# Performance work log

Hardware: AMD Instinct MI355X
Metric: run time of the kernel (lower is better)

The kernel has to match this reference:

```python
import jax, jax.numpy as jnp
import numpy as np

N, E, F_IN, H, C = 10000, 320000, 256, 256, 40


def setup_inputs() -> dict:
    key = jax.random.key(0)
    ks = jax.random.split(key, 12)
    inp = {
        "x": jax.random.normal(ks[0], (N, F_IN), dtype=jnp.float32),
        "edge_index": jax.random.randint(ks[1], (2, E), 0, N, dtype=jnp.int64),
    }
    dims = [(F_IN, H), (H, H), (H, H), (H, H), (H, C)]
    for i, (din, dout) in enumerate(dims, start=1):
        scale = 1.0 / np.sqrt(din)
        inp[f"W{i}"] = jax.random.normal(ks[1 + i], (din, dout), dtype=jnp.float32) * scale
        inp[f"b{i}"] = jnp.zeros((dout,), dtype=jnp.float32)
    return inp


def _gcn_norm(edge_index, num_nodes, dtype):
    # GCNConv: add self-loops, symmetric normalization D^-1/2 (A+I) D^-1/2
    loops = jnp.arange(num_nodes, dtype=edge_index.dtype)
    src = jnp.concatenate([edge_index[0], loops])
    dst = jnp.concatenate([edge_index[1], loops])
    deg = jax.ops.segment_sum(jnp.ones_like(dst, dtype=dtype), dst, num_segments=num_nodes)
    dinv = jnp.where(deg > 0, deg ** -0.5, 0.0).astype(dtype)
    norm = dinv[src] * dinv[dst]  # [E+N]
    return src, dst, norm


def _conv(h, src, dst, norm, W, b, num_nodes):
    # linear transform then gather-scale-scatter aggregation
    h = h @ W                           # [N, dout]
    msg = h[src] * norm[:, None]        # [E+N, dout]
    return jax.ops.segment_sum(msg, dst, num_segments=num_nodes) + b


def reference(x, edge_index, W1, b1, W2, b2, W3, b3, W4, b4, W5, b5):
    num_nodes = x.shape[0]
    src, dst, norm = _gcn_norm(edge_index, num_nodes, x.dtype)
    h = jax.nn.relu(_conv(x, src, dst, norm, W1, b1, num_nodes))
    h = jax.nn.relu(_conv(h, src, dst, norm, W2, b2, num_nodes))
    h = jax.nn.relu(_conv(h, src, dst, norm, W3, b3, num_nodes))
    h = jax.nn.relu(_conv(h, src, dst, norm, W4, b4, num_nodes))
    logits = _conv(h, src, dst, norm, W5, b5, num_nodes)
    return jax.nn.log_softmax(logits, axis=1), logits
```

## Files before the change

kernel.cpp:

```cpp
#include <hip/hip_runtime.h>
#include <hip/hip_bf16.h>

#define N_NODES 10000
#define N_EDGES 320000
#define HDIM    256
#define NCLS    40
#define WTOT    273448

typedef __attribute__((ext_vector_type(8))) short short8;
typedef __attribute__((ext_vector_type(4))) float floatx4;
typedef unsigned long long ull;
typedef unsigned short ushort;

__device__ __forceinline__ float bf2f(ushort u) {
    union { unsigned int i; float f; } v; v.i = ((unsigned int)u) << 16; return v.f;
}
__device__ __forceinline__ ushort f2bf(float f) {
    __hip_bfloat16 h = __float2bfloat16(f);
    return *reinterpret_cast<ushort*>(&h);
}

__device__ __forceinline__ void detect_flags(const void* x, const void* ei,
                                             int* sflags) {
    const int tid = threadIdx.x;
    if (tid < 64) {
        const ushort* u = (const ushort*)x;
        int e = (u[2 * tid] >> 7) & 0xFF;
        ull badmask = __ballot(e < 100 || e > 140);
        const int* ii = (const int*)ei;
        ull oddnz = __ballot(ii[2 * tid + 1] != 0);
        if (tid == 0) {
            sflags[0] = (__popcll(badmask) >= 8) ? 1 : 0;
            sflags[1] = (oddnz == 0) ? 1 : 0;
        }
    }
    __syncthreads();
}


struct PrepArgs {
    const void* x;
    const void* ei;
    const void* wsrc[10];
    ushort* wdst[10];
    int woffs[11];
    ushort* xb;
    int* src32;
    int* dst32;
    int* cnt;
    ushort* tbuf;
    ushort* hbuf;
    int* flags;
};

#define PREP_XB 2500
#define PREP_WB 1069
#define PREP_EB 1250
#define PREP_TOTAL (PREP_XB + PREP_WB + PREP_EB + 1)

__global__ __launch_bounds__(256)
void prep_kernel(PrepArgs a) {
    __shared__ int sflags[2];
    detect_flags(a.x, a.ei, sflags);
    const int f32 = sflags[0];
    const int b = blockIdx.x;

    if (b < PREP_XB) {
        int i4 = b * 256 + threadIdx.x;
        if (f32) {
            float4 v = ((const float4*)a.x)[i4];
            ull p = (ull)f2bf(v.x) | ((ull)f2bf(v.y) << 16) |
                    ((ull)f2bf(v.z) << 32) | ((ull)f2bf(v.w) << 48);
            ((ull*)a.xb)[i4] = p;
        } else {
            ((ull*)a.xb)[i4] = ((const ull*)a.x)[i4];
        }
    } else if (b < PREP_XB + PREP_WB) {
        int i = (b - PREP_XB) * 256 + threadIdx.x;
        if (i < WTOT) {
            int t = 0;
#pragma unroll
            for (int k = 1; k < 10; ++k) t += (i >= a.woffs[k]);
            int local = i - a.woffs[t];
            ushort v;
            if (f32) v = f2bf(((const float*)a.wsrc[t])[local]);
            else     v = ((const ushort*)a.wsrc[t])[local];
            a.wdst[t][local] = v;
        }
    } else if (b < PREP_XB + PREP_WB + PREP_EB) {
        int e = (b - PREP_XB - PREP_WB) * 256 + threadIdx.x;
        const int* ii = (const int*)a.ei;
        int s, d;
        if (sflags[1]) { s = ii[2 * e]; d = ii[2 * (N_EDGES + e)]; }
        else           { s = ii[e];     d = ii[N_EDGES + e]; }
        s = ((unsigned)s < N_NODES) ? s : 0;
        d = ((unsigned)d < N_NODES) ? d : 0;
        a.src32[e] = s;
        a.dst32[e] = d;
        atomicAdd(&a.cnt[d], 1);
    } else {
        int t = threadIdx.x;
        if (t < 64)       ((ull*)(a.tbuf + (size_t)N_NODES * 256))[t] = 0;
        else if (t < 128) ((ull*)(a.hbuf + (size_t)N_NODES * 256))[t - 64] = 0;
        if (t == 0) { a.flags[0] = sflags[0]; a.flags[1] = sflags[1]; }
    }
}


__global__ __launch_bounds__(1024)
void scan_dinv_kernel(const int* __restrict__ cnt, int* __restrict__ offs,
                      int* __restrict__ woff, float* __restrict__ dinv) {
    __shared__ int part[1024];
    const int t = threadIdx.x;
    const int CH = (N_NODES + 1023) / 1024;
    const int base = t * CH;
    int s = 0;
    for (int j = 0; j < CH; ++j) {
        int i = base + j;
        if (i < N_NODES) s += cnt[i];
    }
    part[t] = s;
    __syncthreads();
    for (int off = 1; off < 1024; off <<= 1) {
        int v = 0;
        if (t >= off) v = part[t - off];
        __syncthreads();
        part[t] += v;
        __syncthreads();
    }
    int run = (t == 0) ? 0 : part[t - 1];
    for (int j = 0; j < CH; ++j) {
        int i = base + j;
        if (i < N_NODES) {
            int c = cnt[i];
            offs[i] = run;
            woff[i] = run;
            dinv[i] = rsqrtf((float)c + 1.0f);
            run += c;
        }
    }
}


#define FILL_BLKS 1250
#define GEMM1_YT  78
#define FG_TOTAL  (FILL_BLKS + 8 * GEMM1_YT)

__global__ __launch_bounds__(256)
void fillgemm_kernel(const int* __restrict__ src, const int* __restrict__ dst,
                     int* __restrict__ woff, int* __restrict__ csr,
                     const ushort* __restrict__ A, const ushort* __restrict__ W,
                     const float* __restrict__ dinv, ushort* __restrict__ T) {
    const int b = blockIdx.x;
    if (b < FILL_BLKS) {
        int e = b * 256 + threadIdx.x;
        int d = dst[e];
        int p = atomicAdd(&woff[d], 1);
        csr[p] = src[e];
        return;
    }
    const int g = b - FILL_BLKS;
    const int lane = threadIdx.x & 63;
    const int wave = threadIdx.x >> 6;
    const int m = lane & 15;
    const int quad = lane >> 4;
    const int c0 = (g & 7) * 32;
    const int by = g >> 3;

    short8 bfrag[2][8];
#pragma unroll
    for (int t = 0; t < 2; ++t)
#pragma unroll
        for (int s = 0; s < 8; ++s)
#pragma unroll
            for (int j = 0; j < 8; ++j)
                bfrag[t][s][j] = (short)W[(size_t)(s * 32 + quad * 8 + j) * 256 + c0 + t * 16 + m];

    const int step = GEMM1_YT * 4;
    for (int rt = by * 4 + wave; rt < N_NODES / 16; rt += step) {
        const int r0 = rt * 16;
        floatx4 acc0 = {0.f, 0.f, 0.f, 0.f};
        floatx4 acc1 = {0.f, 0.f, 0.f, 0.f};
        const ushort* arow = A + (size_t)(r0 + m) * 256 + quad * 8;
#pragma unroll
        for (int s = 0; s < 8; ++s) {
            short8 af = *(const short8*)(arow + s * 32);
            acc0 = __builtin_amdgcn_mfma_f32_16x16x32_bf16(af, bfrag[0][s], acc0, 0, 0, 0);
            acc1 = __builtin_amdgcn_mfma_f32_16x16x32_bf16(af, bfrag[1][s], acc1, 0, 0, 0);
        }
#pragma unroll
        for (int r = 0; r < 4; ++r) {
            int row = r0 + quad * 4 + r;
            float di = dinv[row];
            T[(size_t)row * 256 + c0 + m]      = f2bf(acc0[r] * di);
            T[(size_t)row * 256 + c0 + 16 + m] = f2bf(acc1[r] * di);
        }
    }
}


__global__ __launch_bounds__(256)
void gemm256_kernel(const ushort* __restrict__ A, const ushort* __restrict__ W,
                    const float* __restrict__ dinv, ushort* __restrict__ T) {
    const int lane = threadIdx.x & 63;
    const int wave = threadIdx.x >> 6;
    const int m = lane & 15;
    const int quad = lane >> 4;
    const int c0 = blockIdx.x * 32;

    short8 bfrag[2][8];
#pragma unroll
    for (int t = 0; t < 2; ++t)
#pragma unroll
        for (int s = 0; s < 8; ++s)
#pragma unroll
            for (int j = 0; j < 8; ++j)
                bfrag[t][s][j] = (short)W[(size_t)(s * 32 + quad * 8 + j) * 256 + c0 + t * 16 + m];

    const int step = gridDim.y * 4;
    for (int rt = blockIdx.y * 4 + wave; rt < N_NODES / 16; rt += step) {
        const int r0 = rt * 16;
        floatx4 acc0 = {0.f, 0.f, 0.f, 0.f};
        floatx4 acc1 = {0.f, 0.f, 0.f, 0.f};
        const ushort* arow = A + (size_t)(r0 + m) * 256 + quad * 8;
#pragma unroll
        for (int s = 0; s < 8; ++s) {
            short8 af = *(const short8*)(arow + s * 32);
            acc0 = __builtin_amdgcn_mfma_f32_16x16x32_bf16(af, bfrag[0][s], acc0, 0, 0, 0);
            acc1 = __builtin_amdgcn_mfma_f32_16x16x32_bf16(af, bfrag[1][s], acc1, 0, 0, 0);
        }
#pragma unroll
        for (int r = 0; r < 4; ++r) {
            int row = r0 + quad * 4 + r;
            float di = dinv[row];
            T[(size_t)row * 256 + c0 + m]      = f2bf(acc0[r] * di);
            T[(size_t)row * 256 + c0 + 16 + m] = f2bf(acc1[r] * di);
        }
    }
}


__global__ __launch_bounds__(256)
void gemm40_kernel(const ushort* __restrict__ A, const ushort* __restrict__ W,
                   const float* __restrict__ dinv, float* __restrict__ T) {
    const int lane = threadIdx.x & 63;
    const int wave = threadIdx.x >> 6;
    const int m = lane & 15;
    const int quad = lane >> 4;
    const int col = blockIdx.x * 16 + m;
    const bool colok = col < NCLS;

    short8 bfrag[8];
#pragma unroll
    for (int s = 0; s < 8; ++s)
#pragma unroll
        for (int j = 0; j < 8; ++j)
            bfrag[s][j] = colok ? (short)W[(size_t)(s * 32 + quad * 8 + j) * NCLS + col] : (short)0;

    const int step = gridDim.y * 4;
    for (int rt = blockIdx.y * 4 + wave; rt < N_NODES / 16; rt += step) {
        const int r0 = rt * 16;
        floatx4 acc = {0.f, 0.f, 0.f, 0.f};
        const ushort* arow = A + (size_t)(r0 + m) * 256 + quad * 8;
#pragma unroll
        for (int s = 0; s < 8; ++s) {
            short8 af = *(const short8*)(arow + s * 32);
            acc = __builtin_amdgcn_mfma_f32_16x16x32_bf16(af, bfrag[s], acc, 0, 0, 0);
        }
        if (colok) {
#pragma unroll
            for (int r = 0; r < 4; ++r) {
                int row = r0 + quad * 4 + r;
                T[(size_t)row * NCLS + col] = acc[r] * dinv[row];
            }
        }
    }
}


__device__ __forceinline__ void accum16(float* acc, int4 r) {
    int d[4] = {r.x, r.y, r.z, r.w};
#pragma unroll
    for (int k = 0; k < 4; ++k) {
        union { int i; float f; } lo, hi;
        lo.i = d[k] << 16;
        hi.i = d[k] & 0xffff0000;
        acc[2 * k]     += lo.f;
        acc[2 * k + 1] += hi.f;
    }
}

__global__ __launch_bounds__(256)
void agg256_kernel(const ushort* __restrict__ T,
                   const int* __restrict__ csr, const int* __restrict__ offs,
                   const int* __restrict__ cnt, const float* __restrict__ dinv,
                   const ushort* __restrict__ bias,
                   ushort* __restrict__ H) {
    const int node = blockIdx.x * 4 + (threadIdx.x >> 6);
    const int lane = threadIdx.x & 63;
    const int half = lane >> 5;
    const int q = lane & 31;
    const int start = offs[node];
    const int count = cnt[node];
    const float di = dinv[node];

    float acc[8];
    {
        int sinit = half ? N_NODES : node;
        int4 r = *(const int4*)(T + (size_t)sinit * 256 + q * 8);
#pragma unroll
        for (int k = 0; k < 4; ++k) {
            union { int i; float f; } lo, hi;
            int d = (&r.x)[k];
            lo.i = d << 16; hi.i = d & 0xffff0000;
            acc[2 * k] = lo.f; acc[2 * k + 1] = hi.f;
        }
    }

    for (int bj = 0; bj < count; bj += 64) {
        int mrem = count - bj;
        int mm = mrem < 64 ? mrem : 64;
        int idxv = (lane < mm) ? csr[start + bj + lane] : N_NODES;
        int j2 = 0;
        for (; j2 + 8 <= mm; j2 += 8) {
            int s0 = __shfl(idxv, j2 + half);
            int s1 = __shfl(idxv, j2 + 2 + half);
            int s2 = __shfl(idxv, j2 + 4 + half);
            int s3 = __shfl(idxv, j2 + 6 + half);
            int4 r0 = *(const int4*)(T + (size_t)s0 * 256 + q * 8);
            int4 r1 = *(const int4*)(T + (size_t)s1 * 256 + q * 8);
            int4 r2 = *(const int4*)(T + (size_t)s2 * 256 + q * 8);
            int4 r3 = *(const int4*)(T + (size_t)s3 * 256 + q * 8);
            accum16(acc, r0); accum16(acc, r1); accum16(acc, r2); accum16(acc, r3);
        }
        for (; j2 < mm; j2 += 2) {
            int s = __shfl(idxv, j2 + half);
            int4 r = *(const int4*)(T + (size_t)s * 256 + q * 8);
            accum16(acc, r);
        }
    }

#pragma unroll
    for (int i = 0; i < 8; ++i) acc[i] += __shfl_xor(acc[i], 32);

    if (half == 0) {
        int4 bv = *(const int4*)(bias + q * 8);
        int out_d[4];
#pragma unroll
        for (int k = 0; k < 4; ++k) {
            union { int i; float f; } lo, hi;
            int d = (&bv.x)[k];
            lo.i = d << 16; hi.i = d & 0xffff0000;
            float v0 = fmaxf(acc[2 * k] * di + lo.f, 0.f);
            float v1 = fmaxf(acc[2 * k + 1] * di + hi.f, 0.f);
            out_d[k] = (int)f2bf(v0) | ((int)f2bf(v1) << 16);
        }
        *(int4*)(H + (size_t)node * 256 + q * 8) = *(int4*)out_d;
    }
}


__global__ __launch_bounds__(256)
void aggsoft_kernel(const float* __restrict__ T,
                    const int* __restrict__ csr, const int* __restrict__ offs,
                    const int* __restrict__ cnt, const float* __restrict__ dinv,
                    const ushort* __restrict__ bias,
                    void* __restrict__ out, const int* __restrict__ flags) {
    const int node = blockIdx.x * 4 + (threadIdx.x >> 6);
    const int lane = threadIdx.x & 63;
    const int start = offs[node];
    const int count = cnt[node];
    const float di = dinv[node];

    float acc = (lane < NCLS) ? T[(size_t)node * NCLS + lane] : 0.f;
    for (int bj = 0; bj < count; bj += 64) {
        int mrem = count - bj;
        int mm = mrem < 64 ? mrem : 64;
        int idxv = (lane < mm) ? csr[start + bj + lane] : 0;
        int jj = 0;
        for (; jj + 4 <= mm; jj += 4) {
            int s0 = __shfl(idxv, jj + 0);
            int s1 = __shfl(idxv, jj + 1);
            int s2 = __shfl(idxv, jj + 2);
            int s3 = __shfl(idxv, jj + 3);
            if (lane < NCLS) {
                float t0 = T[(size_t)s0 * NCLS + lane];
                float t1 = T[(size_t)s1 * NCLS + lane];
                float t2 = T[(size_t)s2 * NCLS + lane];
                float t3 = T[(size_t)s3 * NCLS + lane];
                acc += t0 + t1 + t2 + t3;
            }
        }
        for (; jj < mm; ++jj) {
            int s = __shfl(idxv, jj);
            if (lane < NCLS) acc += T[(size_t)s * NCLS + lane];
        }
    }

    float l = (lane < NCLS) ? (acc * di + bf2f(bias[lane])) : -INFINITY;
    float mx = l;
#pragma unroll
    for (int o = 32; o > 0; o >>= 1) mx = fmaxf(mx, __shfl_xor(mx, o));
    float e = (lane < NCLS) ? __expf(l - mx) : 0.f;
    float sum = e;
#pragma unroll
    for (int o = 32; o > 0; o >>= 1) sum += __shfl_xor(sum, o);
    float ls = l - mx - __logf(sum);
    if (lane < NCLS) {
        size_t i0 = (size_t)node * NCLS + lane;
        size_t i1 = (size_t)N_NODES * NCLS + i0;
        if (flags[0]) {
            ((float*)out)[i0] = ls;
            ((float*)out)[i1] = l;
        } else {
            ((ushort*)out)[i0] = f2bf(ls);
            ((ushort*)out)[i1] = f2bf(l);
        }
    }
}


static inline size_t alup(size_t x) { return (x + 255) & ~(size_t)255; }

extern "C" void kernel_launch(void* const* d_in, const int* in_sizes, int n_in,
                              void* d_out, int out_size, void* d_ws, size_t ws_size,
                              hipStream_t stream) {
    char* w = (char*)d_ws;
    int* flags   = (int*)w;           w += alup(16);
    float* dinv  = (float*)w;         w += alup(N_NODES * 4);
    int* cnt     = (int*)w;           w += alup(N_NODES * 4);
    int* offs    = (int*)w;           w += alup(N_NODES * 4);
    int* woff    = (int*)w;           w += alup(N_NODES * 4);
    int* src32   = (int*)w;           w += alup(N_EDGES * 4);
    int* dst32   = (int*)w;           w += alup(N_EDGES * 4);
    int* csr     = (int*)w;           w += alup(N_EDGES * 4);
    ushort* xb   = (ushort*)w;        w += alup((size_t)N_NODES * HDIM * 2);
    ushort* wb[5]; ushort* bb[5];
    for (int l = 0; l < 5; ++l) {
        int wn = (l < 4) ? HDIM * HDIM : HDIM * NCLS;
        int bn = (l < 4) ? HDIM : NCLS;
        wb[l] = (ushort*)w; w += alup((size_t)wn * 2);
        bb[l] = (ushort*)w; w += alup((size_t)bn * 2);
    }
    ushort* tbuf = (ushort*)w;        w += alup((size_t)(N_NODES + 16) * HDIM * 2);
    ushort* hbuf = (ushort*)w;        w += alup((size_t)(N_NODES + 16) * HDIM * 2);
    float* t5    = (float*)w;         w += alup((size_t)N_NODES * NCLS * 4);

    hipMemsetAsync(cnt, 0, N_NODES * 4, stream);

    PrepArgs pa;
    pa.x = d_in[0];
    pa.ei = d_in[1];
    int sizes[10] = { HDIM * HDIM, HDIM, HDIM * HDIM, HDIM, HDIM * HDIM, HDIM,
                      HDIM * HDIM, HDIM, HDIM * NCLS, NCLS };
    int run = 0;
    for (int t = 0; t < 10; ++t) {
        pa.wsrc[t] = d_in[2 + t];
        pa.wdst[t] = (t & 1) ? bb[t >> 1] : wb[t >> 1];
        pa.woffs[t] = run;
        run += sizes[t];
    }
    pa.woffs[10] = run;
    pa.xb = xb; pa.src32 = src32; pa.dst32 = dst32; pa.cnt = cnt;
    pa.tbuf = tbuf; pa.hbuf = hbuf; pa.flags = flags;

    prep_kernel<<<PREP_TOTAL, 256, 0, stream>>>(pa);
    scan_dinv_kernel<<<1, 1024, 0, stream>>>(cnt, offs, woff, dinv);
    fillgemm_kernel<<<FG_TOTAL, 256, 0, stream>>>(src32, dst32, woff, csr,
                                                  xb, wb[0], dinv, tbuf);

    const int aggblk = N_NODES / 4;

    agg256_kernel<<<aggblk, 256, 0, stream>>>(tbuf, csr, offs, cnt, dinv, bb[0], hbuf);
    for (int l = 1; l < 4; ++l) {
        gemm256_kernel<<<dim3(8, 78), 256, 0, stream>>>(hbuf, wb[l], dinv, tbuf);
        agg256_kernel<<<aggblk, 256, 0, stream>>>(tbuf, csr, offs, cnt, dinv, bb[l], hbuf);
    }
    gemm40_kernel<<<dim3(3, 80), 256, 0, stream>>>(hbuf, wb[4], dinv, t5);
    aggsoft_kernel<<<aggblk, 256, 0, stream>>>(t5, csr, offs, cnt, dinv, bb[4], d_out, flags);
}
```

Before: 269.1 us.

## Split agg256 feature columns across block pairs with quarter-wave edge gathers

The 256-dim aggregation now splits each node's 256 features into two 128-column halves handled by different blocks, doubling the grid. Each wave processes four edges in parallel per load step (16 lanes per row, 256-byte segments), and the partials are reduced with two xor shuffles. Adjacent block IDs are interleaved so both halves of the same node group run close together, which keeps the gathered rows in L2. The change aims to raise parallelism and memory-level concurrency per wave, at the cost of reading the CSR indices twice and doing an extra shuffle reduction.

```diff
diff --git a/kernel.cpp b/kernel.cpp
--- a/kernel.cpp
+++ b/kernel.cpp
@@ -290,24 +290,32 @@
     }
 }
 
-__global__ __launch_bounds__(256)
+#define AGG_BLKS 5000
+
+__global__ __launch_bounds__(256, 4)
 void agg256_kernel(const ushort* __restrict__ T,
                    const int* __restrict__ csr, const int* __restrict__ offs,
                    const int* __restrict__ cnt, const float* __restrict__ dinv,
                    const ushort* __restrict__ bias,
                    ushort* __restrict__ H) {
-    const int node = blockIdx.x * 4 + (threadIdx.x >> 6);
+    const int bid = blockIdx.x;
+    const int h = (bid >> 2) & 1;
+    const int local = (bid >> 3) * 4 + (bid & 3);
+    const int wave = threadIdx.x >> 6;
+    const int node = local * 4 + wave;
     const int lane = threadIdx.x & 63;
-    const int half = lane >> 5;
-    const int q = lane & 31;
+    const int quarter = lane >> 4;
+    const int q = lane & 15;
+    const int cbase = h * 128 + q * 8;
+
     const int start = offs[node];
     const int count = cnt[node];
     const float di = dinv[node];
 
     float acc[8];
     {
-        int sinit = half ? N_NODES : node;
-        int4 r = *(const int4*)(T + (size_t)sinit * 256 + q * 8);
+        int sinit = quarter ? N_NODES : node;
+        int4 r = *(const int4*)(T + (size_t)sinit * 256 + cbase);
 #pragma unroll
         for (int k = 0; k < 4; ++k) {
             union { int i; float f; } lo, hi;
@@ -322,29 +330,32 @@
         int mm = mrem < 64 ? mrem : 64;
         int idxv = (lane < mm) ? csr[start + bj + lane] : N_NODES;
         int j2 = 0;
-        for (; j2 + 8 <= mm; j2 += 8) {
-            int s0 = __shfl(idxv, j2 + half);
-            int s1 = __shfl(idxv, j2 + 2 + half);
-            int s2 = __shfl(idxv, j2 + 4 + half);
-            int s3 = __shfl(idxv, j2 + 6 + half);
-            int4 r0 = *(const int4*)(T + (size_t)s0 * 256 + q * 8);
-            int4 r1 = *(const int4*)(T + (size_t)s1 * 256 + q * 8);
-            int4 r2 = *(const int4*)(T + (size_t)s2 * 256 + q * 8);
-            int4 r3 = *(const int4*)(T + (size_t)s3 * 256 + q * 8);
+        for (; j2 + 16 <= mm; j2 += 16) {
+            int s0 = __shfl(idxv, j2 + 0  + quarter);
+            int s1 = __shfl(idxv, j2 + 4  + quarter);
+            int s2 = __shfl(idxv, j2 + 8  + quarter);
+            int s3 = __shfl(idxv, j2 + 12 + quarter);
+            int4 r0 = *(const int4*)(T + (size_t)s0 * 256 + cbase);
+            int4 r1 = *(const int4*)(T + (size_t)s1 * 256 + cbase);
+            int4 r2 = *(const int4*)(T + (size_t)s2 * 256 + cbase);
+            int4 r3 = *(const int4*)(T + (size_t)s3 * 256 + cbase);
             accum16(acc, r0); accum16(acc, r1); accum16(acc, r2); accum16(acc, r3);
         }
-        for (; j2 < mm; j2 += 2) {
-            int s = __shfl(idxv, j2 + half);
-            int4 r = *(const int4*)(T + (size_t)s * 256 + q * 8);
+        for (; j2 < mm; j2 += 4) {
+            int s = __shfl(idxv, j2 + quarter);
+            int4 r = *(const int4*)(T + (size_t)s * 256 + cbase);
             accum16(acc, r);
         }
     }
 
 #pragma unroll
-    for (int i = 0; i < 8; ++i) acc[i] += __shfl_xor(acc[i], 32);
-
-    if (half == 0) {
-        int4 bv = *(const int4*)(bias + q * 8);
+    for (int i = 0; i < 8; ++i) {
+        acc[i] += __shfl_xor(acc[i], 32);
+        acc[i] += __shfl_xor(acc[i], 16);
+    }
+
+    if (quarter == 0) {
+        int4 bv = *(const int4*)(bias + cbase);
         int out_d[4];
 #pragma unroll
         for (int k = 0; k < 4; ++k) {
@@ -355,7 +366,7 @@
             float v1 = fmaxf(acc[2 * k + 1] * di + hi.f, 0.f);
             out_d[k] = (int)f2bf(v0) | ((int)f2bf(v1) << 16);
         }
-        *(int4*)(H + (size_t)node * 256 + q * 8) = *(int4*)out_d;
+        *(int4*)(H + (size_t)node * 256 + cbase) = *(int4*)out_d;
     }
 }
 
@@ -469,13 +480,11 @@
     fillgemm_kernel<<<FG_TOTAL, 256, 0, stream>>>(src32, dst32, woff, csr,
                                                   xb, wb[0], dinv, tbuf);
 
-    const int aggblk = N_NODES / 4;
-
-    agg256_kernel<<<aggblk, 256, 0, stream>>>(tbuf, csr, offs, cnt, dinv, bb[0], hbuf);
+    agg256_kernel<<<AGG_BLKS, 256, 0, stream>>>(tbuf, csr, offs, cnt, dinv, bb[0], hbuf);
     for (int l = 1; l < 4; ++l) {
         gemm256_kernel<<<dim3(8, 78), 256, 0, stream>>>(hbuf, wb[l], dinv, tbuf);
-        agg256_kernel<<<aggblk, 256, 0, stream>>>(tbuf, csr, offs, cnt, dinv, bb[l], hbuf);
+        agg256_kernel<<<AGG_BLKS, 256, 0, stream>>>(tbuf, csr, offs, cnt, dinv, bb[l], hbuf);
     }
     gemm40_kernel<<<dim3(3, 80), 256, 0, stream>>>(hbuf, wb[4], dinv, t5);
-    aggsoft_kernel<<<aggblk, 256, 0, stream>>>(t5, csr, offs, cnt, dinv, bb[4], d_out, flags);
-}
+    aggsoft_kernel<<<2500, 256, 0, stream>>>(t5, csr, offs, cnt, dinv, bb[4], d_out, flags);
+}
```

Result: no change. 269.6 us (+0.2%).
